# Optimization experiments

Measured on AMD Instinct MI355X. Metric: run time of the kernel, lower is better.

## Reference

```python
import jax, jax.numpy as jnp
import numpy as np

DIM = 32      # state dim (enc_shape[0])
LDIM = 256    # latent dim (enc_shape[-1])
N_AUX = LDIM // 2
AUX_H = 128   # aux hidden
ENC_H = 256   # encoder hidden
T = 64        # n_shifts
N = 1024      # batch
DT = 0.01


def setup_inputs() -> dict:
    key = jax.random.key(0)
    ks = jax.random.split(key, 13)
    def w(k, shape, fan):
        return jax.random.normal(k, shape, jnp.float32) / np.sqrt(fan).astype(np.float32)
    return {
        "xs": jax.random.normal(ks[0], (N, T, DIM), jnp.float32),
        # encoder MLP: dim -> 256 -> 256 -> ldim (last layer has no bias)
        "enc_W1": w(ks[1], (DIM, ENC_H), DIM), "enc_b1": w(ks[2], (ENC_H,), ENC_H),
        "enc_W2": w(ks[3], (ENC_H, ENC_H), ENC_H), "enc_b2": w(ks[4], (ENC_H,), ENC_H),
        "enc_W3": w(ks[5], (ENC_H, LDIM), ENC_H),
        # n_aux independent aux MLPs: dim -> 128 -> 128 -> 2 (last no bias), stacked
        "aux_W1": w(ks[6], (N_AUX, DIM, AUX_H), DIM), "aux_b1": w(ks[7], (N_AUX, AUX_H), AUX_H),
        "aux_W2": w(ks[8], (N_AUX, AUX_H, AUX_H), AUX_H), "aux_b2": w(ks[9], (N_AUX, AUX_H), AUX_H),
        "aux_W3": w(ks[10], (N_AUX, AUX_H, 2), AUX_H),
        # C: Linear(ldim, dim, bias=False); stored as [ldim, dim] so x_next = y @ C_W
        "C_W": w(ks[11], (LDIM, DIM), LDIM),
    }


def reference(xs, enc_W1, enc_b1, enc_W2, enc_b2, enc_W3,
              aux_W1, aux_b1, aux_W2, aux_b2, aux_W3, C_W):
    x0 = xs[:, 0, :]                                    # [N, dim]
    # all n_aux tiny MLPs batched via einsum (instead of python loop)
    h = jax.nn.relu(jnp.einsum('nd,kdh->nkh', x0, aux_W1) + aux_b1)
    h = jax.nn.relu(jnp.einsum('nkh,khg->nkg', h, aux_W2) + aux_b2)
    aux = jnp.einsum('nkh,kho->nko', h, aux_W3)          # [N, n_aux, 2] -> (mu, omega)
    scale = jnp.exp(aux[..., 0] * DT)
    cos = jnp.cos(aux[..., 1] * DT) * scale              # [N, n_aux]
    sin = jnp.sin(aux[..., 1] * DT) * scale

    # encoder over all n_shifts timesteps
    e = jax.nn.relu(xs @ enc_W1 + enc_b1)
    e = jax.nn.relu(e @ enc_W2 + enc_b2)
    e = e @ enc_W3                                       # [N, T, ldim]
    y = jnp.concatenate([xs, e], axis=-1)                # [N, T, dim+ldim]

    # Koopman recurrence. The original builds a block-diagonal [ldim, ldim]
    # matrix of 2x2 rotation-scaling blocks (block k acts on latent pair
    # (2k, 2k+1)) and applies it as a row-vector bmm: out = y_row @ K with
    # K_block = [[cos, sin], [-sin, cos]]. We apply the blocks directly.
    y0 = e[:, 0, :].reshape(N, N_AUX, 2)
    def step(carry, _):
        y1, y2 = carry[..., 0], carry[..., 1]
        yn = jnp.stack([y1 * cos - y2 * sin, y1 * sin + y2 * cos], axis=-1)
        return yn, yn
    _, ys = jax.lax.scan(step, y0, None, length=T - 1)   # [T-1, N, n_aux, 2]
    ys = jnp.moveaxis(ys, 0, 1).reshape(N, T - 1, LDIM)  # [N, T-1, ldim]

    y_lat = jnp.concatenate([e[:, :1, :], ys], axis=1)          # [N, T, ldim]
    x_pred = jnp.concatenate([xs[:, :1, :], ys @ C_W], axis=1)  # [N, T, dim]
    y_pred = jnp.concatenate([x_pred, y_lat], axis=-1)          # [N, T, dim+ldim]
    return y, y_pred
```

## Files before the change

### kernel.cpp

```cpp
#include <hip/hip_runtime.h>
#include <math.h>

#define N_SEQ 1024
#define T_SEQ 64
#define DIMX  32
#define LDIM  256
#define NAUX  128
#define AUXH  128
#define ENCH  256
#define OUTC  288
#define DT    0.01f

typedef short bf16x8 __attribute__((ext_vector_type(8)));
typedef float f32x4  __attribute__((ext_vector_type(4)));

__device__ __forceinline__ unsigned short f2bf(float f) {
    unsigned u = __builtin_bit_cast(unsigned, f);
    unsigned r = u + 0x7fffu + ((u >> 16) & 1u);
    return (unsigned short)(r >> 16);
}
__device__ __forceinline__ float bf2f(unsigned short h) {
    unsigned u = ((unsigned)h) << 16;
    return __builtin_bit_cast(float, u);
}
__device__ __forceinline__ f32x4 mfma16(bf16x8 a, bf16x8 b, f32x4 c) {
    return __builtin_amdgcn_mfma_f32_16x16x32_bf16(a, b, c, 0, 0, 0);
}

#define CV_ENC   139264
#define PREP_CONV_BLOCKS 576
__global__ __launch_bounds__(256) void prep_kernel(
    const float* __restrict__ eW1, const float* __restrict__ eW2,
    const float* __restrict__ eW3, const float* __restrict__ C_W,
    const float* __restrict__ aW1, const float* __restrict__ aW2,
    unsigned short* __restrict__ encw, float* __restrict__ cwt,
    unsigned short* __restrict__ a1h, unsigned short* __restrict__ a1l,
    unsigned short* __restrict__ a2h, unsigned short* __restrict__ a2l)
{
    __shared__ float tile[32][33];
    const int b   = blockIdx.x;
    const int tid = threadIdx.x;

    if (b < PREP_CONV_BLOCKS) {
        const int idx = b * 256 + tid;
        if (idx < 8192) {
            int c = idx >> 5, k = idx & 31;
            encw[idx] = f2bf(eW1[k * ENCH + c]);
        } else if (idx < 8192 + 65536) {
            int t = idx - 8192; int c = t >> 8, k = t & 255;
            encw[idx] = f2bf(eW2[k * ENCH + c]);
        } else if (idx < CV_ENC) {
            int t = idx - (8192 + 65536); int c = t >> 8, k = t & 255;
            encw[idx] = f2bf(eW3[k * LDIM + c]);
        } else if (idx < CV_ENC + 8192) {
            int t = idx - CV_ENC; int d = t >> 8, l = t & 255;
            cwt[t] = C_W[l * DIMX + d];
        }
        return;
    }

    const int bb0 = b - PREP_CONV_BLOCKS;
    const float* src; unsigned short *dh, *dl; int R, j0, r0;
    if (bb0 < 512) {
        int k = bb0 >> 2; j0 = (bb0 & 3) * 32; r0 = 0; R = 32;
        src = aW1 + (size_t)k * 4096;
        dh = a1h + (size_t)k * 4096; dl = a1l + (size_t)k * 4096;
    } else {
        int bb = bb0 - 512;
        int k = bb >> 4; j0 = ((bb >> 2) & 3) * 32; r0 = (bb & 3) * 32; R = 128;
        src = aW2 + (size_t)k * 16384;
        dh = a2h + (size_t)k * 16384; dl = a2l + (size_t)k * 16384;
    }

    for (int i = tid; i < 1024; i += 256) {
        int rr = i >> 5, jj = i & 31;
        tile[rr][jj] = src[(r0 + rr) * 128 + j0 + jj];
    }
    __syncthreads();
    for (int i = tid; i < 1024; i += 256) {
        int jj = i >> 5, rr = i & 31;
        float w = tile[rr][jj];
        unsigned short hi = f2bf(w);
        int off = (j0 + jj) * R + r0 + rr;
        dh[off] = hi;
        dl[off] = f2bf(w - bf2f(hi));
    }
}

__global__ __launch_bounds__(256) void auxm_kernel(
    const float* __restrict__ xs,
    const unsigned short* __restrict__ W1h, const unsigned short* __restrict__ W1l,
    const float* __restrict__ b1,
    const unsigned short* __restrict__ W2h, const unsigned short* __restrict__ W2l,
    const float* __restrict__ b2,
    const float* __restrict__ W3,
    float* __restrict__ a_ws, float* __restrict__ th_ws)
{
    const int k   = blockIdx.x >> 4;
    const int n0  = (blockIdx.x & 15) << 6;
    const int tid = threadIdx.x;
    const int wv  = tid >> 6;
    const int ln  = tid & 63;
    const int lr  = ln & 15;
    const int g   = ln >> 4;
    const int cb  = wv * 32;

    __shared__ unsigned short x0h[64][40];
    __shared__ unsigned short x0l[64][40];
    __shared__ unsigned short h1h[64][136];
    __shared__ unsigned short h1l[64][136];
    __shared__ float          p3[256];

    for (int i = tid; i < 512; i += 256) {
        int r = i >> 3, qd = i & 7;
        float4 v = *(const float4*)&xs[(size_t)(n0 + r) * (T_SEQ * DIMX) + qd * 4];
        short4 hs, ls;
        float vv[4] = {v.x, v.y, v.z, v.w};
        short* hp = (short*)&hs; short* lp = (short*)&ls;
        #pragma unroll
        for (int u = 0; u < 4; ++u) {
            unsigned short hi = f2bf(vv[u]);
            hp[u] = (short)hi;
            lp[u] = (short)f2bf(vv[u] - bf2f(hi));
        }
        *(short4*)&x0h[r][qd * 4] = hs;
        *(short4*)&x0l[r][qd * 4] = ls;
    }
    __syncthreads();

    {
        const unsigned short* W1hk = W1h + (size_t)k * 4096;
        const unsigned short* W1lk = W1l + (size_t)k * 4096;
        bf16x8 bh[2], bl[2];
        #pragma unroll
        for (int ct = 0; ct < 2; ++ct) {
            int off = (cb + ct * 16 + lr) * 32 + g * 8;
            bh[ct] = *(const bf16x8*)&W1hk[off];
            bl[ct] = *(const bf16x8*)&W1lk[off];
        }
        f32x4 acc[4][2];
        #pragma unroll
        for (int rt = 0; rt < 4; ++rt) {
            bf16x8 ah = *(const bf16x8*)&x0h[rt * 16 + lr][g * 8];
            bf16x8 al = *(const bf16x8*)&x0l[rt * 16 + lr][g * 8];
            #pragma unroll
            for (int ct = 0; ct < 2; ++ct) {
                f32x4 z = {0.f, 0.f, 0.f, 0.f};
                z = mfma16(ah, bl[ct], z);
                z = mfma16(al, bh[ct], z);
                acc[rt][ct] = mfma16(ah, bh[ct], z);
            }
        }
        #pragma unroll
        for (int ct = 0; ct < 2; ++ct) {
            const int col = cb + ct * 16 + lr;
            const float bb = b1[k * 128 + col];
            #pragma unroll
            for (int rt = 0; rt < 4; ++rt)
                #pragma unroll
                for (int i = 0; i < 4; ++i) {
                    float h = fmaxf(acc[rt][ct][i] + bb, 0.f);
                    unsigned short hi = f2bf(h);
                    int row = rt * 16 + g * 4 + i;
                    h1h[row][col] = hi;
                    h1l[row][col] = f2bf(h - bf2f(hi));
                }
        }
    }
    __syncthreads();

    {
        const unsigned short* W2hk = W2h + (size_t)k * 16384;
        const unsigned short* W2lk = W2l + (size_t)k * 16384;
        f32x4 acc[4][2];
        #pragma unroll
        for (int rt = 0; rt < 4; ++rt)
            #pragma unroll
            for (int ct = 0; ct < 2; ++ct) acc[rt][ct] = (f32x4){0.f,0.f,0.f,0.f};

        #pragma unroll
        for (int kk = 0; kk < 4; ++kk) {
            bf16x8 bh[2], bl[2], ah[4], al[4];
            #pragma unroll
            for (int ct = 0; ct < 2; ++ct) {
                int off = (cb + ct * 16 + lr) * 128 + kk * 32 + g * 8;
                bh[ct] = *(const bf16x8*)&W2hk[off];
                bl[ct] = *(const bf16x8*)&W2lk[off];
            }
            #pragma unroll
            for (int rt = 0; rt < 4; ++rt) {
                ah[rt] = *(const bf16x8*)&h1h[rt * 16 + lr][kk * 32 + g * 8];
                al[rt] = *(const bf16x8*)&h1l[rt * 16 + lr][kk * 32 + g * 8];
            }
            #pragma unroll
            for (int rt = 0; rt < 4; ++rt)
                #pragma unroll
                for (int ct = 0; ct < 2; ++ct) {
                    f32x4 z = acc[rt][ct];
                    z = mfma16(ah[rt], bl[ct], z);
                    z = mfma16(al[rt], bh[ct], z);
                    acc[rt][ct] = mfma16(ah[rt], bh[ct], z);
                }
        }
        __syncthreads();
        #pragma unroll
        for (int ct = 0; ct < 2; ++ct) {
            const int col = cb + ct * 16 + lr;
            const float bb = b2[k * 128 + col];
            #pragma unroll
            for (int rt = 0; rt < 4; ++rt)
                #pragma unroll
                for (int i = 0; i < 4; ++i) {
                    float h = fmaxf(acc[rt][ct][i] + bb, 0.f);
                    unsigned short hi = f2bf(h);
                    int row = rt * 16 + g * 4 + i;
                    h1h[row][col] = hi;
                    h1l[row][col] = f2bf(h - bf2f(hi));
                }
        }
    }
    __syncthreads();

    {
        const int hh = tid >> 7, r = tid & 127, n = r >> 1, o = r & 1;
        const float* W3k = W3 + (size_t)k * (AUXH * 2);
        float s = 0.f;
        #pragma unroll
        for (int h8 = hh * 64; h8 < hh * 64 + 64; h8 += 8) {
            bf16x8 vh = *(const bf16x8*)&h1h[n][h8];
            bf16x8 vl = *(const bf16x8*)&h1l[n][h8];
            #pragma unroll
            for (int u = 0; u < 8; ++u) {
                float hv = bf2f((unsigned short)vh[u]) + bf2f((unsigned short)vl[u]);
                s += hv * W3k[(h8 + u) * 2 + o];
            }
        }
        p3[tid] = s;
    }
    __syncthreads();
    if (tid < 128) {
        const int n = tid >> 1, o = tid & 1;
        float v = (p3[tid] + p3[tid + 128]) * DT;
        float* dst = o ? th_ws : a_ws;
        dst[(size_t)(n0 + n) * NAUX + k] = v;
    }
}

__global__ __launch_bounds__(256) void encm_kernel(
    const float* __restrict__ xs,
    const unsigned short* __restrict__ W1T, const float* __restrict__ b1,
    const unsigned short* __restrict__ W2T, const float* __restrict__ b2,
    const unsigned short* __restrict__ W3T,
    float* __restrict__ y)
{
    __shared__ float          Xf[64 * 36];
    __shared__ unsigned short Hs[64 * 264];

    const int tid = threadIdx.x;
    const int wv  = tid >> 6;
    const int ln  = tid & 63;
    const int lr  = ln & 15;
    const int g   = ln >> 4;
    const int cb  = wv * 64;
    const size_t row0 = (size_t)blockIdx.x * 64;

    {
        const float4* src = (const float4*)(xs + row0 * DIMX);
        for (int i = tid; i < 512; i += 256) {
            int r = i >> 3, q = i & 7;
            *(float4*)&Xf[r * 36 + q * 4] = src[i];
        }
    }
    __syncthreads();

    {
        f32x4 acc[4][4];
        bf16x8 bfr[4], afr[4];
        #pragma unroll
        for (int ct = 0; ct < 4; ++ct)
            bfr[ct] = *(const bf16x8*)&W1T[(cb + ct * 16 + lr) * 32 + g * 8];
        #pragma unroll
        for (int rt = 0; rt < 4; ++rt) {
            const float* xp = &Xf[(rt * 16 + lr) * 36 + g * 8];
            float4 u = *(const float4*)xp;
            float4 v = *(const float4*)(xp + 4);
            bf16x8 t;
            t[0]=(short)f2bf(u.x); t[1]=(short)f2bf(u.y); t[2]=(short)f2bf(u.z); t[3]=(short)f2bf(u.w);
            t[4]=(short)f2bf(v.x); t[5]=(short)f2bf(v.y); t[6]=(short)f2bf(v.z); t[7]=(short)f2bf(v.w);
            afr[rt] = t;
        }
        #pragma unroll
        for (int rt = 0; rt < 4; ++rt)
            #pragma unroll
            for (int ct = 0; ct < 4; ++ct) {
                f32x4 z = {0.f, 0.f, 0.f, 0.f};
                acc[rt][ct] = mfma16(afr[rt], bfr[ct], z);
            }
        #pragma unroll
        for (int ct = 0; ct < 4; ++ct) {
            const float bb = b1[cb + ct * 16 + lr];
            #pragma unroll
            for (int rt = 0; rt < 4; ++rt)
                #pragma unroll
                for (int i = 0; i < 4; ++i) {
                    float h = fmaxf(acc[rt][ct][i] + bb, 0.f);
                    Hs[(rt * 16 + g * 4 + i) * 264 + cb + ct * 16 + lr] = f2bf(h);
                }
        }
    }
    __syncthreads();

    int wrow[4], hoff[4];
    #pragma unroll
    for (int ct = 0; ct < 4; ++ct) wrow[ct] = (cb + ct * 16 + lr) * 256 + g * 8;
    #pragma unroll
    for (int rt = 0; rt < 4; ++rt) hoff[rt] = (rt * 16 + lr) * 264 + g * 8;

    {
        f32x4 acc[4][4];
        #pragma unroll
        for (int rt = 0; rt < 4; ++rt)
            #pragma unroll
            for (int ct = 0; ct < 4; ++ct) acc[rt][ct] = (f32x4){0.f,0.f,0.f,0.f};
        #pragma unroll 2
        for (int kk = 0; kk < 8; ++kk) {
            bf16x8 bfr[4], afr[4];
            #pragma unroll
            for (int ct = 0; ct < 4; ++ct)
                bfr[ct] = *(const bf16x8*)&W2T[wrow[ct] + kk * 32];
            #pragma unroll
            for (int rt = 0; rt < 4; ++rt)
                afr[rt] = *(const bf16x8*)&Hs[hoff[rt] + kk * 32];
            #pragma unroll
            for (int rt = 0; rt < 4; ++rt)
                #pragma unroll
                for (int ct = 0; ct < 4; ++ct)
                    acc[rt][ct] = mfma16(afr[rt], bfr[ct], acc[rt][ct]);
        }
        __syncthreads();
        #pragma unroll
        for (int ct = 0; ct < 4; ++ct) {
            const float bb = b2[cb + ct * 16 + lr];
            #pragma unroll
            for (int rt = 0; rt < 4; ++rt)
                #pragma unroll
                for (int i = 0; i < 4; ++i) {
                    float h = fmaxf(acc[rt][ct][i] + bb, 0.f);
                    Hs[(rt * 16 + g * 4 + i) * 264 + cb + ct * 16 + lr] = f2bf(h);
                }
        }
    }
    __syncthreads();

    {
        f32x4 acc[4][4];
        #pragma unroll
        for (int rt = 0; rt < 4; ++rt)
            #pragma unroll
            for (int ct = 0; ct < 4; ++ct) acc[rt][ct] = (f32x4){0.f,0.f,0.f,0.f};
        #pragma unroll 2
        for (int kk = 0; kk < 8; ++kk) {
            bf16x8 bfr[4], afr[4];
            #pragma unroll
            for (int ct = 0; ct < 4; ++ct)
                bfr[ct] = *(const bf16x8*)&W3T[wrow[ct] + kk * 32];
            #pragma unroll
            for (int rt = 0; rt < 4; ++rt)
                afr[rt] = *(const bf16x8*)&Hs[hoff[rt] + kk * 32];
            #pragma unroll
            for (int rt = 0; rt < 4; ++rt)
                #pragma unroll
                for (int ct = 0; ct < 4; ++ct)
                    acc[rt][ct] = mfma16(afr[rt], bfr[ct], acc[rt][ct]);
        }
        #pragma unroll
        for (int ct = 0; ct < 4; ++ct) {
            const int c3 = cb + ct * 16 + lr;
            #pragma unroll
            for (int rt = 0; rt < 4; ++rt)
                #pragma unroll
                for (int i = 0; i < 4; ++i)
                    y[(row0 + rt * 16 + g * 4 + i) * OUTC + DIMX + c3] = acc[rt][ct][i];
        }
    }

    for (int i = tid; i < 512; i += 256) {
        int r = i >> 3, q = i & 7;
        *(float4*)&y[(row0 + r) * OUTC + q * 4] = *(const float4*)&Xf[r * 36 + q * 4];
    }
}

__global__ __launch_bounds__(256) void enc0_kernel(
    const float* __restrict__ xs,
    const float* __restrict__ W1, const float* __restrict__ b1,
    const float* __restrict__ W2, const float* __restrict__ b2,
    const float* __restrict__ W3,
    float* __restrict__ y)
{
    __shared__ float Xs[4 * 32];
    __shared__ float Hsf[4 * 256];
    const int tid = threadIdx.x;
    const int c   = tid;
    const int n0  = blockIdx.x * 4;

    if (tid < 32) {
        int r = tid >> 3, q = tid & 7;
        *(float4*)&Xs[r * 32 + q * 4] =
            *(const float4*)&xs[(size_t)(n0 + r) * (T_SEQ * DIMX) + q * 4];
    }
    __syncthreads();

    float acc[4];
    {
        float w[32];
        #pragma unroll
        for (int d = 0; d < 32; ++d) w[d] = W1[d * ENCH + c];
        const float bb = b1[c];
        #pragma unroll
        for (int r = 0; r < 4; ++r) {
            float a = bb;
            #pragma unroll
            for (int d4 = 0; d4 < 8; ++d4) {
                float4 xv = *(const float4*)&Xs[r * 32 + d4 * 4];
                a += xv.x * w[d4*4] + xv.y * w[d4*4+1] + xv.z * w[d4*4+2] + xv.w * w[d4*4+3];
            }
            acc[r] = a;
        }
        #pragma unroll
        for (int r = 0; r < 4; ++r) Hsf[r * 256 + c] = fmaxf(acc[r], 0.f);
    }
    __syncthreads();
    {
        const float bb = b2[c];
        #pragma unroll
        for (int r = 0; r < 4; ++r) acc[r] = bb;
        for (int hc = 0; hc < 8; ++hc) {
            float w[32];
            #pragma unroll
            for (int i = 0; i < 32; ++i) w[i] = W2[(hc * 32 + i) * ENCH + c];
            #pragma unroll
            for (int r = 0; r < 4; ++r) {
                float a = acc[r];
                #pragma unroll
                for (int h4 = 0; h4 < 8; ++h4) {
                    float4 hv = *(const float4*)&Hsf[r * 256 + hc * 32 + h4 * 4];
                    a += hv.x * w[h4*4] + hv.y * w[h4*4+1] + hv.z * w[h4*4+2] + hv.w * w[h4*4+3];
                }
                acc[r] = a;
            }
        }
        __syncthreads();
        #pragma unroll
        for (int r = 0; r < 4; ++r) Hsf[r * 256 + c] = fmaxf(acc[r], 0.f);
    }
    __syncthreads();
    {
        #pragma unroll
        for (int r = 0; r < 4; ++r) acc[r] = 0.f;
        for (int hc = 0; hc < 8; ++hc) {
            float w[32];
            #pragma unroll
            for (int i = 0; i < 32; ++i) w[i] = W3[(hc * 32 + i) * LDIM + c];
            #pragma unroll
            for (int r = 0; r < 4; ++r) {
                float a = acc[r];
                #pragma unroll
                for (int h4 = 0; h4 < 8; ++h4) {
                    float4 hv = *(const float4*)&Hsf[r * 256 + hc * 32 + h4 * 4];
                    a += hv.x * w[h4*4] + hv.y * w[h4*4+1] + hv.z * w[h4*4+2] + hv.w * w[h4*4+3];
                }
                acc[r] = a;
            }
        }
    }
    #pragma unroll
    for (int r = 0; r < 4; ++r)
        y[((size_t)(n0 + r) * T_SEQ) * OUTC + DIMX + c] = acc[r];
}

__global__ __launch_bounds__(256) void scan3_kernel(
    const float* __restrict__ xs,
    const float* __restrict__ a_ws, const float* __restrict__ th_ws,
    const float* __restrict__ cwt,
    const float* __restrict__ y,
    float* __restrict__ yp)
{
    __shared__ float ys_lds[16][256];

    const int n = blockIdx.x >> 2;
    const int q = blockIdx.x & 3;
    const int e = threadIdx.x;
    const int k = e >> 1;

    const float* yrow0 = y + (size_t)n * T_SEQ * OUTC + DIMX;
    float2 y0 = *(const float2*)&yrow0[e & ~1];
    const float a  = a_ws [n * NAUX + k];
    const float th = th_ws[n * NAUX + k];

    const float m = expf(a);
    float ss, cc; sincosf(th, &ss, &cc);
    const float zr = m * cc, zi = m * ss;

    float pr = zr, pi = zi;
    #pragma unroll
    for (int s2 = 0; s2 < 4; ++s2) {
        float nr = pr * pr - pi * pi;
        pi = 2.f * pr * pi; pr = nr;
    }
    float wr = 1.f, wi = 0.f;
    for (int j = 0; j < q; ++j) {
        float nr = wr * pr - wi * pi;
        wi = wr * pi + wi * pr; wr = nr;
    }

    const bool imag = e & 1;
    float* ypn = yp + (size_t)n * T_SEQ * OUTC;

    #pragma unroll 4
    for (int tl = 0; tl < 16; ++tl) {
        const int t = q * 16 + tl;
        float val = imag ? (y0.x * wi + y0.y * wr)
                         : (y0.x * wr - y0.y * wi);
        ypn[(size_t)t * OUTC + DIMX + e] = val;
        ys_lds[tl][(e + ((tl >> 1) & 7) * 4) & 255] = val;
        float nwr = wr * zr - wi * zi;
        wi = wr * zi + wi * zr;
        wr = nwr;
    }
    __syncthreads();

    const int d  = e >> 3;
    const int tg = e & 7;
    const float* cwd = cwt + d * 256;
    const int rot = tg * 4;

    #pragma unroll
    for (int s = 0; s < 2; ++s) {
        const int tl = tg * 2 + s;
        const int t  = q * 16 + tl;
        float o;
        if (t == 0) {
            o = xs[(size_t)n * T_SEQ * DIMX + d];
        } else {
            float sum = 0.f;
            #pragma unroll 8
            for (int l = 0; l < 256; l += 4) {
                const int c0 = (l + rot) & 255;
                float4 yv = *(const float4*)&ys_lds[tl][c0];
                float4 wv = *(const float4*)&cwd[l];
                sum += yv.x * wv.x + yv.y * wv.y + yv.z * wv.z + yv.w * wv.w;
            }
            o = sum;
        }
        ypn[(size_t)t * OUTC + d] = o;
    }
}

extern "C" void kernel_launch(void* const* d_in, const int* in_sizes, int n_in,
                              void* d_out, int out_size, void* d_ws, size_t ws_size,
                              hipStream_t stream)
{
    const float* xs   = (const float*)d_in[0];
    const float* eW1  = (const float*)d_in[1];
    const float* eb1  = (const float*)d_in[2];
    const float* eW2  = (const float*)d_in[3];
    const float* eb2  = (const float*)d_in[4];
    const float* eW3  = (const float*)d_in[5];
    const float* aW1  = (const float*)d_in[6];
    const float* ab1  = (const float*)d_in[7];
    const float* aW2  = (const float*)d_in[8];
    const float* ab2  = (const float*)d_in[9];
    const float* aW3  = (const float*)d_in[10];
    const float* C_W  = (const float*)d_in[11];

    float* y  = (float*)d_out;
    float* yp = y + (size_t)N_SEQ * T_SEQ * OUTC;

    float* a_ws  = (float*)d_ws;
    float* th_ws = a_ws + (size_t)N_SEQ * NAUX;
    unsigned short* encw = (unsigned short*)(th_ws + (size_t)N_SEQ * NAUX);
    unsigned short* W1T = encw;
    unsigned short* W2T = encw + 8192;
    unsigned short* W3T = encw + 8192 + 65536;
    unsigned short* a1h = encw + CV_ENC;
    unsigned short* a1l = a1h + 524288;
    unsigned short* a2h = a1l + 524288;
    unsigned short* a2l = a2h + 2097152;
    float* cwt = (float*)(a2l + 2097152);

    prep_kernel<<<PREP_CONV_BLOCKS + 2560, 256, 0, stream>>>(
        eW1, eW2, eW3, C_W, aW1, aW2, encw, cwt, a1h, a1l, a2h, a2l);
    auxm_kernel <<<128 * 16, 256, 0, stream>>>(
        xs, a1h, a1l, ab1, a2h, a2l, ab2, aW3, a_ws, th_ws);
    encm_kernel <<<N_SEQ * T_SEQ / 64, 256, 0, stream>>>(xs, W1T, eb1, W2T, eb2, W3T, y);
    enc0_kernel <<<N_SEQ / 4, 256, 0, stream>>>(xs, eW1, eb1, eW2, eb2, eW3, y);
    scan3_kernel<<<N_SEQ * 4, 256, 0, stream>>>(xs, a_ws, th_ws, cwt, y, yp);
}
```

Baseline: 190.9 us.

## Stage encoder output through LDS for coalesced stores; simplify enc0 and scan3 projection

The encoder MFMA kernel now stages its accumulator tiles in shared memory and writes full output rows (x passthrough plus latent) with float4 stores, replacing scattered scalar stores. The fp32 t=0 encoder kernel now uses one sample per block with simple loops instead of four samples with register-blocked weights. The scan kernel's C projection computes both timesteps in one loop, sharing each weight load. The trade-offs are extra barriers and LDS reuse in the encoder kernel, and in enc0 four times as many blocks with no weight reuse across samples.

```diff
diff --git a/kernel.cpp b/kernel.cpp
--- a/kernel.cpp
+++ b/kernel.cpp
@@ -373,20 +373,35 @@
                 for (int ct = 0; ct < 4; ++ct)
                     acc[rt][ct] = mfma16(afr[rt], bfr[ct], acc[rt][ct]);
         }
-        #pragma unroll
-        for (int ct = 0; ct < 4; ++ct) {
-            const int c3 = cb + ct * 16 + lr;
-            #pragma unroll
-            for (int rt = 0; rt < 4; ++rt)
-                #pragma unroll
-                for (int i = 0; i < 4; ++i)
-                    y[(row0 + rt * 16 + g * 4 + i) * OUTC + DIMX + c3] = acc[rt][ct][i];
-        }
-    }
-
-    for (int i = tid; i < 512; i += 256) {
-        int r = i >> 3, q = i & 7;
-        *(float4*)&y[(row0 + r) * OUTC + q * 4] = *(const float4*)&Xf[r * 36 + q * 4];
+        __syncthreads();
+
+        float* HsF = (float*)Hs;
+        const int r  = tid >> 3;
+        const int ce = tid & 7;
+
+        #pragma unroll
+        for (int p = 0; p < 2; ++p) {
+            #pragma unroll
+            for (int rt = 2 * p; rt < 2 * p + 2; ++rt)
+                #pragma unroll
+                for (int ct = 0; ct < 4; ++ct)
+                    #pragma unroll
+                    for (int i = 0; i < 4; ++i)
+                        HsF[((rt - 2 * p) * 16 + g * 4 + i) * 264 + cb + ct * 16 + lr]
+                            = acc[rt][ct][i];
+            __syncthreads();
+            const int rloc = p * 32 + r;
+            float* dstrow = &y[(row0 + rloc) * OUTC];
+            #pragma unroll
+            for (int j = 0; j < 9; ++j) {
+                int f4 = j * 8 + ce;
+                float4 v;
+                if (f4 < 8) v = *(const float4*)&Xf[rloc * 36 + f4 * 4];
+                else        v = *(const float4*)&HsF[r * 264 + (f4 - 8) * 4];
+                *(float4*)&dstrow[f4 * 4] = v;
+            }
+            __syncthreads();
+        }
     }
 }
 
@@ -397,85 +412,35 @@
     const float* __restrict__ W3,
     float* __restrict__ y)
 {
-    __shared__ float Xs[4 * 32];
-    __shared__ float Hsf[4 * 256];
+    __shared__ float Xs[32];
+    __shared__ float Hsf[256];
     const int tid = threadIdx.x;
     const int c   = tid;
-    const int n0  = blockIdx.x * 4;
-
-    if (tid < 32) {
-        int r = tid >> 3, q = tid & 7;
-        *(float4*)&Xs[r * 32 + q * 4] =
-            *(const float4*)&xs[(size_t)(n0 + r) * (T_SEQ * DIMX) + q * 4];
-    }
-    __syncthreads();
-
-    float acc[4];
-    {
-        float w[32];
-        #pragma unroll
-        for (int d = 0; d < 32; ++d) w[d] = W1[d * ENCH + c];
-        const float bb = b1[c];
-        #pragma unroll
-        for (int r = 0; r < 4; ++r) {
-            float a = bb;
-            #pragma unroll
-            for (int d4 = 0; d4 < 8; ++d4) {
-                float4 xv = *(const float4*)&Xs[r * 32 + d4 * 4];
-                a += xv.x * w[d4*4] + xv.y * w[d4*4+1] + xv.z * w[d4*4+2] + xv.w * w[d4*4+3];
-            }
-            acc[r] = a;
-        }
-        #pragma unroll
-        for (int r = 0; r < 4; ++r) Hsf[r * 256 + c] = fmaxf(acc[r], 0.f);
-    }
-    __syncthreads();
-    {
-        const float bb = b2[c];
-        #pragma unroll
-        for (int r = 0; r < 4; ++r) acc[r] = bb;
-        for (int hc = 0; hc < 8; ++hc) {
-            float w[32];
-            #pragma unroll
-            for (int i = 0; i < 32; ++i) w[i] = W2[(hc * 32 + i) * ENCH + c];
-            #pragma unroll
-            for (int r = 0; r < 4; ++r) {
-                float a = acc[r];
-                #pragma unroll
-                for (int h4 = 0; h4 < 8; ++h4) {
-                    float4 hv = *(const float4*)&Hsf[r * 256 + hc * 32 + h4 * 4];
-                    a += hv.x * w[h4*4] + hv.y * w[h4*4+1] + hv.z * w[h4*4+2] + hv.w * w[h4*4+3];
-                }
-                acc[r] = a;
-            }
-        }
-        __syncthreads();
-        #pragma unroll
-        for (int r = 0; r < 4; ++r) Hsf[r * 256 + c] = fmaxf(acc[r], 0.f);
-    }
-    __syncthreads();
-    {
-        #pragma unroll
-        for (int r = 0; r < 4; ++r) acc[r] = 0.f;
-        for (int hc = 0; hc < 8; ++hc) {
-            float w[32];
-            #pragma unroll
-            for (int i = 0; i < 32; ++i) w[i] = W3[(hc * 32 + i) * LDIM + c];
-            #pragma unroll
-            for (int r = 0; r < 4; ++r) {
-                float a = acc[r];
-                #pragma unroll
-                for (int h4 = 0; h4 < 8; ++h4) {
-                    float4 hv = *(const float4*)&Hsf[r * 256 + hc * 32 + h4 * 4];
-                    a += hv.x * w[h4*4] + hv.y * w[h4*4+1] + hv.z * w[h4*4+2] + hv.w * w[h4*4+3];
-                }
-                acc[r] = a;
-            }
-        }
-    }
-    #pragma unroll
-    for (int r = 0; r < 4; ++r)
-        y[((size_t)(n0 + r) * T_SEQ) * OUTC + DIMX + c] = acc[r];
+    const int n   = blockIdx.x;
+
+    if (tid < 32) Xs[tid] = xs[(size_t)n * (T_SEQ * DIMX) + tid];
+    __syncthreads();
+
+    float a = b1[c];
+    #pragma unroll 8
+    for (int d = 0; d < 32; ++d)
+        a += Xs[d] * W1[d * ENCH + c];
+    Hsf[c] = fmaxf(a, 0.f);
+    __syncthreads();
+
+    float a2 = b2[c];
+    #pragma unroll 8
+    for (int h = 0; h < 256; ++h)
+        a2 += Hsf[h] * W2[h * ENCH + c];
+    __syncthreads();
+    Hsf[c] = fmaxf(a2, 0.f);
+    __syncthreads();
+
+    float a3 = 0.f;
+    #pragma unroll 8
+    for (int h = 0; h < 256; ++h)
+        a3 += Hsf[h] * W3[h * LDIM + c];
+    y[((size_t)n * T_SEQ) * OUTC + DIMX + c] = a3;
 }
 
 __global__ __launch_bounds__(256) void scan3_kernel(
@@ -529,31 +494,27 @@
     }
     __syncthreads();
 
-    const int d  = e >> 3;
-    const int tg = e & 7;
+    const int d   = e >> 3;
+    const int tg  = e & 7;
+    const int tl0 = tg * 2, tl1 = tl0 + 1;
     const float* cwd = cwt + d * 256;
     const int rot = tg * 4;
 
-    #pragma unroll
-    for (int s = 0; s < 2; ++s) {
-        const int tl = tg * 2 + s;
-        const int t  = q * 16 + tl;
-        float o;
-        if (t == 0) {
-            o = xs[(size_t)n * T_SEQ * DIMX + d];
-        } else {
-            float sum = 0.f;
-            #pragma unroll 8
-            for (int l = 0; l < 256; l += 4) {
-                const int c0 = (l + rot) & 255;
-                float4 yv = *(const float4*)&ys_lds[tl][c0];
-                float4 wv = *(const float4*)&cwd[l];
-                sum += yv.x * wv.x + yv.y * wv.y + yv.z * wv.z + yv.w * wv.w;
-            }
-            o = sum;
-        }
-        ypn[(size_t)t * OUTC + d] = o;
-    }
+    float s0 = 0.f, s1 = 0.f;
+    #pragma unroll 8
+    for (int l = 0; l < 256; l += 4) {
+        const int c0 = (l + rot) & 255;
+        float4 wv = *(const float4*)&cwd[l];
+        float4 ya = *(const float4*)&ys_lds[tl0][c0];
+        float4 yb = *(const float4*)&ys_lds[tl1][c0];
+        s0 += ya.x * wv.x + ya.y * wv.y + ya.z * wv.z + ya.w * wv.w;
+        s1 += yb.x * wv.x + yb.y * wv.y + yb.z * wv.z + yb.w * wv.w;
+    }
+    const int t0 = q * 16 + tl0;
+    const int t1 = q * 16 + tl1;
+    float o0 = (t0 == 0) ? xs[(size_t)n * T_SEQ * DIMX + d] : s0;
+    ypn[(size_t)t0 * OUTC + d] = o0;
+    ypn[(size_t)t1 * OUTC + d] = s1;
 }
 
 extern "C" void kernel_launch(void* const* d_in, const int* in_sizes, int n_in,
@@ -593,6 +554,6 @@
     auxm_kernel <<<128 * 16, 256, 0, stream>>>(
         xs, a1h, a1l, ab1, a2h, a2l, ab2, aW3, a_ws, th_ws);
     encm_kernel <<<N_SEQ * T_SEQ / 64, 256, 0, stream>>>(xs, W1T, eb1, W2T, eb2, W3T, y);
-    enc0_kernel <<<N_SEQ / 4, 256, 0, stream>>>(xs, eW1, eb1, eW2, eb2, eW3, y);
+    enc0_kernel <<<N_SEQ, 256, 0, stream>>>(xs, eW1, eb1, eW2, eb2, eW3, y);
     scan3_kernel<<<N_SEQ * 4, 256, 0, stream>>>(xs, a_ws, th_ws, cwt, y, yp);
 }
```

After: 161.2 us. 1.18x faster.
